# Optimization experiments

Measured on AMD Instinct MI355X. Metric: run time of the kernel, lower is better.

The kernel has to match this reference:

```python
import jax, jax.numpy as jnp
import numpy as np

N_NODES = 100000
N_EDGES = 1600000
D_IN = 128
D_HID = 128
N_GRAPHS = 128


def setup_inputs() -> dict:
    key = jax.random.key(0)
    ks = jax.random.split(key, 6)
    x = jax.random.normal(ks[0], (N_NODES, D_IN), dtype=jnp.float32)
    edge_index = jax.random.randint(ks[1], (2, N_EDGES), 0, N_NODES, dtype=jnp.int32)
    batch = jnp.sort(jax.random.randint(ks[2], (N_NODES,), 0, N_GRAPHS, dtype=jnp.int32))
    # GCNConv params (glorot-ish weight, zero bias), PReLU slope init 0.25 per channel
    W = jax.random.normal(ks[3], (D_IN, D_HID), dtype=jnp.float32) / np.float32(np.sqrt(D_IN))
    b = jnp.zeros((D_HID,), dtype=jnp.float32)
    prelu_a = jnp.full((D_HID,), 0.25, dtype=jnp.float32)
    return {"x": x, "edge_index": edge_index, "batch": batch, "W": W, "b": b, "prelu_a": prelu_a}


def reference(x, edge_index, batch, W, b, prelu_a):
    n_nodes = x.shape[0]
    # ---- GCNConv: add self-loops, symmetric deg^-1/2 normalization ----
    h = x @ W  # [N, H]
    loop = jnp.arange(n_nodes, dtype=edge_index.dtype)
    src = jnp.concatenate([edge_index[0], loop])  # [E+N]
    dst = jnp.concatenate([edge_index[1], loop])
    deg = jax.ops.segment_sum(jnp.ones_like(dst, jnp.float32), dst, num_segments=n_nodes)
    dinv = jnp.where(deg > 0, jax.lax.rsqrt(deg), 0.0)  # deg^-1/2 (inf -> 0, as in PyG)
    norm = dinv[src] * dinv[dst]  # [E+N]
    msg = h[src] * norm[:, None]  # gather + scale
    out = jax.ops.segment_sum(msg, dst, num_segments=n_nodes) + b  # scatter-add
    # ---- PReLU (per-channel slope) ----
    out = jnp.where(out > 0, out, prelu_a * out)
    # ---- F.normalize: L2 over dim=1, eps=1e-12 ----
    nrm = jnp.sqrt(jnp.sum(out * out, axis=1, keepdims=True))
    out = out / jnp.maximum(nrm, 1e-12)
    # ---- global_mean_pool over batch ids ----
    cnt = jax.ops.segment_sum(jnp.ones((n_nodes,), jnp.float32), batch, num_segments=N_GRAPHS)
    pooled = jax.ops.segment_sum(out, batch, num_segments=N_GRAPHS) / jnp.maximum(cnt, 1.0)[:, None]
    return pooled  # [N_GRAPHS, D_HID]
```

## Files before the change

### kernel.cpp

```cpp
#include <hip/hip_runtime.h>

#define D 128
#define NG 128
#define CAP 64
#define BIN 128
#define EPB 4096
#define NBMAX 1024

typedef unsigned short ushort_t;
typedef __bf16 bf16x8 __attribute__((ext_vector_type(8)));
typedef float floatx4 __attribute__((ext_vector_type(4)));

static __device__ __forceinline__ unsigned short f2bf(float f) {
    unsigned u = __float_as_uint(f);
    unsigned r = (u + 0x7fffu + ((u >> 16) & 1u)) >> 16;
    return (unsigned short)r;
}
static __device__ __forceinline__ void acc2(float2& a, unsigned v) {
    a.x += __uint_as_float(v << 16);
    a.y += __uint_as_float(v & 0xffff0000u);
}

__global__ __launch_bounds__(256) void k_init(const float* __restrict__ W, ushort_t* __restrict__ Wp,
                                              const int* __restrict__ batch, int N,
                                              float* __restrict__ cntinv, float* __restrict__ out,
                                              int* __restrict__ cursor, int nb, int cap,
                                              ushort_t* __restrict__ h) {
    int t = blockIdx.x * 256 + threadIdx.x;
    int T = gridDim.x * 256;
    for (int i = t; i < NG * D; i += T) out[i] = 0.f;
    for (int b = t; b < nb; b += T) cursor[b] = b * cap;
    for (int i = t; i < D; i += T) h[(size_t)N * D + i] = 0;
    if (blockIdx.x == 0) {
        int tid = threadIdx.x;
        for (int i = tid; i < D * D; i += 256) {
            int c = i >> 7, k = i & 127;
            Wp[i] = f2bf(W[k * D + c]);
        }
        if (tid < NG) {
            int g = tid;
            int lo = 0, hi = N;
            while (lo < hi) { int mid = (lo + hi) >> 1; if (batch[mid] < g) lo = mid + 1; else hi = mid; }
            int a = lo;
            hi = N;
            while (lo < hi) { int mid = (lo + hi) >> 1; if (batch[mid] < g + 1) lo = mid + 1; else hi = mid; }
            int c = lo - a;
            cntinv[g] = 1.0f / (float)(c > 1 ? c : 1);
        }
    }
}

__global__ __launch_bounds__(256) void k_ascatter(const int* __restrict__ src, const int* __restrict__ dst,
                                                  int E, int nb, int* __restrict__ cursor,
                                                  int* __restrict__ ebuf) {
    __shared__ int hist[NBMAX];
    __shared__ int curs[NBMAX];
    int tid = threadIdx.x;
    for (int i = tid; i < nb; i += 256) hist[i] = 0;
    __syncthreads();
    int base = blockIdx.x * EPB;
    int cnt = E - base; if (cnt > EPB) cnt = EPB;
    for (int k = tid; k < cnt; k += 256) {
        atomicAdd(&hist[(unsigned)dst[base + k] >> 7], 1);
    }
    __syncthreads();
    for (int i = tid; i < nb; i += 256) {
        int v = hist[i];
        curs[i] = v ? atomicAdd(&cursor[i], v) : 0;
    }
    __syncthreads();
    for (int k = tid; k < cnt; k += 256) {
        int dv = dst[base + k];
        int sv = src[base + k];
        int pos = atomicAdd(&curs[dv >> 7], 1);
        ebuf[pos] = (sv << 7) | ((dv & 127) << 24);
    }
}

__global__ __launch_bounds__(512) void k_bucket(int* __restrict__ ebuf, const int* __restrict__ cursor,
                                                int cap, int N, int* __restrict__ rs, int* __restrict__ deg) {
    __shared__ int lists[BIN * CAP];
    __shared__ int lcnt[BIN];
    __shared__ int lpos[BIN];
    int tid = threadIdx.x;
    int b = blockIdx.x;
    if (tid < BIN) lcnt[tid] = 0;
    __syncthreads();
    int s = b * cap;
    int e = cursor[b];
    for (int i = s + tid; i < e; i += 512) {
        int pk = ebuf[i];
        int n = (unsigned)pk >> 24;
        int pos = atomicAdd(&lcnt[n], 1);
        if (pos < CAP) lists[n * CAP + pos] = pk & 0xFFFFFF;
    }
    __syncthreads();
    int c0 = 0, cp0 = 0;
    if (tid < BIN) {
        c0 = min(lcnt[tid], CAP);
        cp0 = (c0 + 7) & ~7;
        lpos[tid] = cp0;
    }
    __syncthreads();
    for (int off = 1; off < BIN; off <<= 1) {
        int tv = 0;
        if (tid < BIN && tid >= off) tv = lpos[tid - off];
        __syncthreads();
        if (tid < BIN) lpos[tid] += tv;
        __syncthreads();
    }
    int n0 = b * BIN;
    if (tid < BIN) {
        int node = n0 + tid;
        if (node < N) { rs[node] = s + lpos[tid] - cp0; deg[node] = c0; }
    }
    __syncthreads();
    {
        int n = tid >> 2, hf = tid & 3;
        int c = min(lcnt[n], CAP);
        int cp = (c + 7) & ~7;
        int wbase = s + lpos[n] - cp;
        for (int k = hf; k < cp; k += 4) {
            ebuf[wbase + k] = (k < c) ? (lists[n * CAP + k] << 1) : (N << 8);
        }
    }
}

__global__ __launch_bounds__(256) void k_gemm(const float* __restrict__ x, const ushort_t* __restrict__ Wp,
                                              const int* __restrict__ deg, ushort_t* __restrict__ h, int N) {
    __shared__ ushort_t smem[64 * 132 + 128 * 128];
    ushort_t* xs = smem;
    ushort_t* ws = smem + 64 * 132;

    const int tid = threadIdx.x;
    const int w = tid >> 6;
    const int lane = tid & 63;
    const int q = lane >> 4;
    const int m = lane & 15;
    const int row0 = blockIdx.x * 64;

#pragma unroll
    for (int it = 0; it < 8; ++it) {
        int i = it * 256 + tid;
        int r = i >> 5, s = i & 31;
        int row = row0 + r;
        uint2 pk;
        if (row < N) {
            float4 v = *(const float4*)&x[(size_t)row * D + s * 4];
            pk.x = (unsigned)f2bf(v.x) | ((unsigned)f2bf(v.y) << 16);
            pk.y = (unsigned)f2bf(v.z) | ((unsigned)f2bf(v.w) << 16);
        } else {
            pk.x = 0; pk.y = 0;
        }
        int off = (s * 8) ^ ((r & 7) << 4);
        *(uint2*)((char*)xs + r * 256 + off) = pk;
    }
#pragma unroll
    for (int it = 0; it < 8; ++it) {
        int i = it * 256 + tid;
        int c = i >> 4, s = i & 15;
        bf16x8 v = *(const bf16x8*)(Wp + (size_t)c * D + s * 8);
        int off = (s * 16) ^ ((c & 7) << 4);
        *(bf16x8*)((char*)ws + c * 256 + off) = v;
    }
    __syncthreads();

    floatx4 acc[8];
#pragma unroll
    for (int nt = 0; nt < 8; ++nt) acc[nt] = (floatx4){0.f, 0.f, 0.f, 0.f};

    const int arow_l = w * 16 + m;
    const int swz = (m & 7) << 4;
#pragma unroll
    for (int kb = 0; kb < 4; ++kb) {
        const int koff = (kb * 64 + q * 16) ^ swz;
        const bf16x8 av = *(const bf16x8*)((const char*)xs + arow_l * 256 + koff);
#pragma unroll
        for (int nt = 0; nt < 8; ++nt) {
            int c = nt * 16 + m;
            const bf16x8 bv = *(const bf16x8*)((const char*)ws + c * 256 + koff);
            acc[nt] = __builtin_amdgcn_mfma_f32_16x16x32_bf16(av, bv, acc[nt], 0, 0, 0);
        }
    }

    float di[4];
#pragma unroll
    for (int r = 0; r < 4; ++r) {
        int row = row0 + w * 16 + q * 4 + r;
        di[r] = (row < N) ? rsqrtf((float)(deg[row] + 1)) : 0.f;
    }
    __syncthreads();

#pragma unroll
    for (int nt = 0; nt < 8; ++nt) {
#pragma unroll
        for (int r = 0; r < 4; ++r) {
            xs[(w * 16 + q * 4 + r) * 132 + nt * 16 + m] = f2bf(acc[nt][r] * di[r]);
        }
    }
    __syncthreads();
#pragma unroll
    for (int it = 0; it < 8; ++it) {
        int i = it * 256 + tid;
        int r = i >> 5, s = i & 31;
        int row = row0 + r;
        if (row < N) {
            *(uint2*)&h[(size_t)row * D + s * 4] = *(const uint2*)&xs[r * 132 + s * 4];
        }
    }
}

__global__ __launch_bounds__(256) void k_gather(const ushort_t* __restrict__ h,
                                                const int* __restrict__ rs, const int* __restrict__ deg,
                                                const int* __restrict__ ebuf,
                                                const int* __restrict__ batch, const float* __restrict__ b,
                                                const float* __restrict__ pa, const float* __restrict__ cntinv,
                                                float* __restrict__ out, int N) {
    __shared__ float rows[8][128];
    __shared__ int gids[8];
    const int wave = threadIdx.x >> 6;
    const int lane = threadIdx.x & 63;
    const int half = lane >> 5;
    const int fl = lane & 31;
    const int hb = half << 5;
    const int node = blockIdx.x * 8 + wave * 2 + half;
    const bool valid = (node < N);
    const int nodeC = valid ? node : (N - 1);
    const char* hp = (const char*)h;
    const unsigned flb = (unsigned)fl * 8;

    float2 a01 = {0.f, 0.f}, a23 = {0.f, 0.f};

    int start = rs[nodeC];
    int len = valid ? deg[nodeC] : 0;
    int lenp = (len + 7) & ~7;

    unsigned idxA = (fl < lenp) ? (unsigned)ebuf[start + fl] : 0;
    int j1 = lenp < 32 ? lenp : 32;
    for (int j = 0; j < j1; j += 8) {
        unsigned o0 = __shfl(idxA, hb + j + 0) + flb;
        unsigned o1 = __shfl(idxA, hb + j + 1) + flb;
        unsigned o2 = __shfl(idxA, hb + j + 2) + flb;
        unsigned o3 = __shfl(idxA, hb + j + 3) + flb;
        unsigned o4 = __shfl(idxA, hb + j + 4) + flb;
        unsigned o5 = __shfl(idxA, hb + j + 5) + flb;
        unsigned o6 = __shfl(idxA, hb + j + 6) + flb;
        unsigned o7 = __shfl(idxA, hb + j + 7) + flb;
        uint2 v0 = *(const uint2*)(hp + o0);
        uint2 v1 = *(const uint2*)(hp + o1);
        uint2 v2 = *(const uint2*)(hp + o2);
        uint2 v3 = *(const uint2*)(hp + o3);
        uint2 v4 = *(const uint2*)(hp + o4);
        uint2 v5 = *(const uint2*)(hp + o5);
        uint2 v6 = *(const uint2*)(hp + o6);
        uint2 v7 = *(const uint2*)(hp + o7);
        acc2(a01, v0.x); acc2(a23, v0.y);
        acc2(a01, v1.x); acc2(a23, v1.y);
        acc2(a01, v2.x); acc2(a23, v2.y);
        acc2(a01, v3.x); acc2(a23, v3.y);
        acc2(a01, v4.x); acc2(a23, v4.y);
        acc2(a01, v5.x); acc2(a23, v5.y);
        acc2(a01, v6.x); acc2(a23, v6.y);
        acc2(a01, v7.x); acc2(a23, v7.y);
    }
    if (lenp > 32) {
        unsigned idxB = (32 + fl < lenp) ? (unsigned)ebuf[start + 32 + fl] : 0;
        for (int j = 32; j < lenp; j += 8) {
            unsigned o0 = __shfl(idxB, hb + j - 32 + 0) + flb;
            unsigned o1 = __shfl(idxB, hb + j - 32 + 1) + flb;
            unsigned o2 = __shfl(idxB, hb + j - 32 + 2) + flb;
            unsigned o3 = __shfl(idxB, hb + j - 32 + 3) + flb;
            unsigned o4 = __shfl(idxB, hb + j - 32 + 4) + flb;
            unsigned o5 = __shfl(idxB, hb + j - 32 + 5) + flb;
            unsigned o6 = __shfl(idxB, hb + j - 32 + 6) + flb;
            unsigned o7 = __shfl(idxB, hb + j - 32 + 7) + flb;
            uint2 v0 = *(const uint2*)(hp + o0);
            uint2 v1 = *(const uint2*)(hp + o1);
            uint2 v2 = *(const uint2*)(hp + o2);
            uint2 v3 = *(const uint2*)(hp + o3);
            uint2 v4 = *(const uint2*)(hp + o4);
            uint2 v5 = *(const uint2*)(hp + o5);
            uint2 v6 = *(const uint2*)(hp + o6);
            uint2 v7 = *(const uint2*)(hp + o7);
            acc2(a01, v0.x); acc2(a23, v0.y);
            acc2(a01, v1.x); acc2(a23, v1.y);
            acc2(a01, v2.x); acc2(a23, v2.y);
            acc2(a01, v3.x); acc2(a23, v3.y);
            acc2(a01, v4.x); acc2(a23, v4.y);
            acc2(a01, v5.x); acc2(a23, v5.y);
            acc2(a01, v6.x); acc2(a23, v6.y);
            acc2(a01, v7.x); acc2(a23, v7.y);
        }
    }

    uint2 sv = *(const uint2*)(hp + (unsigned)nodeC * 256 + flb);
    acc2(a01, sv.x); acc2(a23, sv.y);

    float dinv = rsqrtf((float)(len + 1));
    float4 bb = *(const float4*)&b[fl * 4];
    float4 aa = *(const float4*)&pa[fl * 4];
    float v0 = a01.x * dinv + bb.x;
    float v1 = a01.y * dinv + bb.y;
    float v2 = a23.x * dinv + bb.z;
    float v3 = a23.y * dinv + bb.w;
    v0 = v0 > 0.f ? v0 : aa.x * v0;
    v1 = v1 > 0.f ? v1 : aa.y * v1;
    v2 = v2 > 0.f ? v2 : aa.z * v2;
    v3 = v3 > 0.f ? v3 : aa.w * v3;
    float ss = v0 * v0 + v1 * v1 + v2 * v2 + v3 * v3;
#pragma unroll
    for (int o = 16; o > 0; o >>= 1) ss += __shfl_xor(ss, o);
    float inv = valid ? (1.0f / fmaxf(sqrtf(ss), 1e-12f)) : 0.f;

    *(float4*)&rows[wave * 2 + half][fl * 4] = make_float4(v0 * inv, v1 * inv, v2 * inv, v3 * inv);
    if (fl == 0) gids[wave * 2 + half] = valid ? batch[node] : -1;
    __syncthreads();

    if (threadIdx.x < 128) {
        int f = threadIdx.x;
        float acc = rows[0][f];
        int g = gids[0];
#pragma unroll
        for (int i = 1; i < 8; ++i) {
            int gi = gids[i];
            float vv = rows[i][f];
            if (gi == g) {
                acc += vv;
            } else {
                if (g >= 0) atomicAdd(&out[(size_t)g * D + f], acc * cntinv[g]);
                g = gi;
                acc = vv;
            }
        }
        if (g >= 0) atomicAdd(&out[(size_t)g * D + f], acc * cntinv[g]);
    }
}

extern "C" void kernel_launch(void* const* d_in, const int* in_sizes, int n_in,
                              void* d_out, int out_size, void* d_ws, size_t ws_size,
                              hipStream_t stream) {
    const float* x = (const float*)d_in[0];
    const int* ei = (const int*)d_in[1];
    const int* batch = (const int*)d_in[2];
    const float* W = (const float*)d_in[3];
    const float* b = (const float*)d_in[4];
    const float* pa = (const float*)d_in[5];
    float* out = (float*)d_out;

    const int N = in_sizes[0] / D;
    const int E = in_sizes[1] / 2;
    const int* src = ei;
    const int* dst = ei + E;

    const int nb = (N + BIN - 1) / BIN;
    const int nblk = (E + EPB - 1) / EPB;
    const int mean = (E + nb - 1) / nb;
    const int cap = mean + mean / 2 + 640;

    char* w = (char*)d_ws;
    auto carve = [&](size_t bytes) {
        void* p = (void*)w;
        w += (bytes + 255) & ~(size_t)255;
        return p;
    };
    ushort_t* h = (ushort_t*)carve((size_t)(N + 1) * D * sizeof(ushort_t));
    ushort_t* Wp = (ushort_t*)carve((size_t)D * D * sizeof(ushort_t));
    int* deg = (int*)carve((size_t)N * sizeof(int));
    int* rs = (int*)carve((size_t)N * sizeof(int));
    int* ebuf = (int*)carve((size_t)nb * cap * sizeof(int));
    int* cursor = (int*)carve(NBMAX * sizeof(int));
    float* cntinv = (float*)carve(NG * sizeof(float));

    k_init<<<32, 256, 0, stream>>>(W, Wp, batch, N, cntinv, out, cursor, nb, cap, h);
    k_ascatter<<<nblk, 256, 0, stream>>>(src, dst, E, nb, cursor, ebuf);
    k_bucket<<<nb, 512, 0, stream>>>(ebuf, cursor, cap, N, rs, deg);
    k_gemm<<<(N + 63) / 64, 256, 0, stream>>>(x, Wp, deg, h, N);
    k_gather<<<(N + 7) / 8, 256, 0, stream>>>(h, rs, deg, ebuf, batch, b, pa, cntinv, out, N);
}
```

Measured before the change: 223.2 us.

## Fuse bucket sort and GEMM into one kernel, compute degrees via atomics

Degree counting moves into the edge-scatter pass through global atomics, so the GEMM no longer depends on the bucket kernel. The bucket and GEMM work are then merged into a single launch, with blocks interleaved between the two roles, letting them overlap. The gather loop is unrolled to 16 loads per step, and the gather is split into two launches. The cost is 1.6M extra global atomics on deg and larger shared-memory pressure for the bucket blocks, which now run 256 threads instead of 512.

```diff
diff --git a/kernel.cpp b/kernel.cpp
--- a/kernel.cpp
+++ b/kernel.cpp
@@ -24,10 +24,11 @@
 __global__ __launch_bounds__(256) void k_init(const float* __restrict__ W, ushort_t* __restrict__ Wp,
                                               const int* __restrict__ batch, int N,
                                               float* __restrict__ cntinv, float* __restrict__ out,
-                                              int* __restrict__ cursor, int nb, int cap,
-                                              ushort_t* __restrict__ h) {
+                                              int* __restrict__ cursor, int* __restrict__ deg,
+                                              int nb, int cap, ushort_t* __restrict__ h) {
     int t = blockIdx.x * 256 + threadIdx.x;
     int T = gridDim.x * 256;
+    for (int i = t; i < N; i += T) deg[i] = 0;
     for (int i = t; i < NG * D; i += T) out[i] = 0.f;
     for (int b = t; b < nb; b += T) cursor[b] = b * cap;
     for (int i = t; i < D; i += T) h[(size_t)N * D + i] = 0;
@@ -52,7 +53,7 @@
 
 __global__ __launch_bounds__(256) void k_ascatter(const int* __restrict__ src, const int* __restrict__ dst,
                                                   int E, int nb, int* __restrict__ cursor,
-                                                  int* __restrict__ ebuf) {
+                                                  int* __restrict__ ebuf, int* __restrict__ deg) {
     __shared__ int hist[NBMAX];
     __shared__ int curs[NBMAX];
     int tid = threadIdx.x;
@@ -61,7 +62,9 @@
     int base = blockIdx.x * EPB;
     int cnt = E - base; if (cnt > EPB) cnt = EPB;
     for (int k = tid; k < cnt; k += 256) {
-        atomicAdd(&hist[(unsigned)dst[base + k] >> 7], 1);
+        int dv = dst[base + k];
+        atomicAdd(&hist[(unsigned)dv >> 7], 1);
+        atomicAdd(&deg[dv], 1);
     }
     __syncthreads();
     for (int i = tid; i < nb; i += 256) {
@@ -77,135 +80,139 @@
     }
 }
 
-__global__ __launch_bounds__(512) void k_bucket(int* __restrict__ ebuf, const int* __restrict__ cursor,
-                                                int cap, int N, int* __restrict__ rs, int* __restrict__ deg) {
-    __shared__ int lists[BIN * CAP];
-    __shared__ int lcnt[BIN];
-    __shared__ int lpos[BIN];
-    int tid = threadIdx.x;
-    int b = blockIdx.x;
-    if (tid < BIN) lcnt[tid] = 0;
-    __syncthreads();
-    int s = b * cap;
-    int e = cursor[b];
-    for (int i = s + tid; i < e; i += 512) {
-        int pk = ebuf[i];
-        int n = (unsigned)pk >> 24;
-        int pos = atomicAdd(&lcnt[n], 1);
-        if (pos < CAP) lists[n * CAP + pos] = pk & 0xFFFFFF;
-    }
-    __syncthreads();
-    int c0 = 0, cp0 = 0;
-    if (tid < BIN) {
-        c0 = min(lcnt[tid], CAP);
-        cp0 = (c0 + 7) & ~7;
-        lpos[tid] = cp0;
-    }
-    __syncthreads();
-    for (int off = 1; off < BIN; off <<= 1) {
-        int tv = 0;
-        if (tid < BIN && tid >= off) tv = lpos[tid - off];
-        __syncthreads();
-        if (tid < BIN) lpos[tid] += tv;
-        __syncthreads();
-    }
-    int n0 = b * BIN;
-    if (tid < BIN) {
-        int node = n0 + tid;
-        if (node < N) { rs[node] = s + lpos[tid] - cp0; deg[node] = c0; }
-    }
-    __syncthreads();
-    {
-        int n = tid >> 2, hf = tid & 3;
-        int c = min(lcnt[n], CAP);
-        int cp = (c + 7) & ~7;
-        int wbase = s + lpos[n] - cp;
-        for (int k = hf; k < cp; k += 4) {
-            ebuf[wbase + k] = (k < c) ? (lists[n * CAP + k] << 1) : (N << 8);
-        }
-    }
-}
-
-__global__ __launch_bounds__(256) void k_gemm(const float* __restrict__ x, const ushort_t* __restrict__ Wp,
-                                              const int* __restrict__ deg, ushort_t* __restrict__ h, int N) {
-    __shared__ ushort_t smem[64 * 132 + 128 * 128];
-    ushort_t* xs = smem;
-    ushort_t* ws = smem + 64 * 132;
-
+__global__ __launch_bounds__(256) void k_mid(const float* __restrict__ x, const ushort_t* __restrict__ Wp,
+                                             const int* __restrict__ deg, ushort_t* __restrict__ h,
+                                             int* __restrict__ ebuf, const int* __restrict__ cursor,
+                                             int cap, int* __restrict__ rs, int N,
+                                             int nbBucket, int total) {
+    __shared__ __align__(16) char smemraw[(64 * 132 + 128 * 128) * 2];
     const int tid = threadIdx.x;
-    const int w = tid >> 6;
-    const int lane = tid & 63;
-    const int q = lane >> 4;
-    const int m = lane & 15;
-    const int row0 = blockIdx.x * 64;
-
-#pragma unroll
-    for (int it = 0; it < 8; ++it) {
-        int i = it * 256 + tid;
-        int r = i >> 5, s = i & 31;
-        int row = row0 + r;
-        uint2 pk;
-        if (row < N) {
-            float4 v = *(const float4*)&x[(size_t)row * D + s * 4];
-            pk.x = (unsigned)f2bf(v.x) | ((unsigned)f2bf(v.y) << 16);
-            pk.y = (unsigned)f2bf(v.z) | ((unsigned)f2bf(v.w) << 16);
-        } else {
-            pk.x = 0; pk.y = 0;
-        }
-        int off = (s * 8) ^ ((r & 7) << 4);
-        *(uint2*)((char*)xs + r * 256 + off) = pk;
-    }
-#pragma unroll
-    for (int it = 0; it < 8; ++it) {
-        int i = it * 256 + tid;
-        int c = i >> 4, s = i & 15;
-        bf16x8 v = *(const bf16x8*)(Wp + (size_t)c * D + s * 8);
-        int off = (s * 16) ^ ((c & 7) << 4);
-        *(bf16x8*)((char*)ws + c * 256 + off) = v;
-    }
-    __syncthreads();
-
-    floatx4 acc[8];
-#pragma unroll
-    for (int nt = 0; nt < 8; ++nt) acc[nt] = (floatx4){0.f, 0.f, 0.f, 0.f};
-
-    const int arow_l = w * 16 + m;
-    const int swz = (m & 7) << 4;
-#pragma unroll
-    for (int kb = 0; kb < 4; ++kb) {
-        const int koff = (kb * 64 + q * 16) ^ swz;
-        const bf16x8 av = *(const bf16x8*)((const char*)xs + arow_l * 256 + koff);
+    const int idx = blockIdx.x;
+    const int bIdx = (int)(((long)idx * nbBucket) / total);
+    const bool isB = (((long)(idx + 1) * nbBucket) / total) > bIdx;
+
+    if (isB) {
+        int* lists = (int*)smemraw;
+        int* lcnt = lists + BIN * CAP;
+        int* lpos = lcnt + BIN;
+        int b = bIdx;
+        if (tid < BIN) lcnt[tid] = 0;
+        __syncthreads();
+        int s = b * cap;
+        int e = cursor[b];
+        for (int i = s + tid; i < e; i += 256) {
+            int pk = ebuf[i];
+            int n = (unsigned)pk >> 24;
+            int pos = atomicAdd(&lcnt[n], 1);
+            if (pos < CAP) lists[n * CAP + pos] = pk & 0xFFFFFF;
+        }
+        __syncthreads();
+        int c0 = 0, cp0 = 0;
+        if (tid < BIN) {
+            c0 = min(lcnt[tid], CAP);
+            cp0 = (c0 + 7) & ~7;
+            lpos[tid] = cp0;
+        }
+        __syncthreads();
+        for (int off = 1; off < BIN; off <<= 1) {
+            int tv = 0;
+            if (tid < BIN && tid >= off) tv = lpos[tid - off];
+            __syncthreads();
+            if (tid < BIN) lpos[tid] += tv;
+            __syncthreads();
+        }
+        int n0 = b * BIN;
+        if (tid < BIN) {
+            int node = n0 + tid;
+            if (node < N) rs[node] = s + lpos[tid] - cp0;
+        }
+        __syncthreads();
+        {
+            int n = tid >> 1, hf = tid & 1;
+            int c = min(lcnt[n], CAP);
+            int cp = (c + 7) & ~7;
+            int wbase = s + lpos[n] - cp;
+            for (int k = hf; k < cp; k += 2) {
+                ebuf[wbase + k] = (k < c) ? (lists[n * CAP + k] << 1) : (N << 8);
+            }
+        }
+    } else {
+        ushort_t* xs = (ushort_t*)smemraw;
+        ushort_t* ws = (ushort_t*)smemraw + 64 * 132;
+        const int w = tid >> 6;
+        const int lane = tid & 63;
+        const int q = lane >> 4;
+        const int m = lane & 15;
+        const int row0 = (idx - bIdx) * 64;
+
+#pragma unroll
+        for (int it = 0; it < 8; ++it) {
+            int i = it * 256 + tid;
+            int r = i >> 5, s = i & 31;
+            int row = row0 + r;
+            uint2 pk;
+            if (row < N) {
+                float4 v = *(const float4*)&x[(size_t)row * D + s * 4];
+                pk.x = (unsigned)f2bf(v.x) | ((unsigned)f2bf(v.y) << 16);
+                pk.y = (unsigned)f2bf(v.z) | ((unsigned)f2bf(v.w) << 16);
+            } else {
+                pk.x = 0; pk.y = 0;
+            }
+            int off = (s * 8) ^ ((r & 7) << 4);
+            *(uint2*)((char*)xs + r * 256 + off) = pk;
+        }
+#pragma unroll
+        for (int it = 0; it < 8; ++it) {
+            int i = it * 256 + tid;
+            int c = i >> 4, s = i & 15;
+            bf16x8 v = *(const bf16x8*)(Wp + (size_t)c * D + s * 8);
+            int off = (s * 16) ^ ((c & 7) << 4);
+            *(bf16x8*)((char*)ws + c * 256 + off) = v;
+        }
+        __syncthreads();
+
+        floatx4 acc[8];
+#pragma unroll
+        for (int nt = 0; nt < 8; ++nt) acc[nt] = (floatx4){0.f, 0.f, 0.f, 0.f};
+
+        const int arow_l = w * 16 + m;
+        const int swz = (m & 7) << 4;
+#pragma unroll
+        for (int kb = 0; kb < 4; ++kb) {
+            const int koff = (kb * 64 + q * 16) ^ swz;
+            const bf16x8 av = *(const bf16x8*)((const char*)xs + arow_l * 256 + koff);
+#pragma unroll
+            for (int nt = 0; nt < 8; ++nt) {
+                int c = nt * 16 + m;
+                const bf16x8 bv = *(const bf16x8*)((const char*)ws + c * 256 + koff);
+                acc[nt] = __builtin_amdgcn_mfma_f32_16x16x32_bf16(av, bv, acc[nt], 0, 0, 0);
+            }
+        }
+
+        float di[4];
+#pragma unroll
+        for (int r = 0; r < 4; ++r) {
+            int row = row0 + w * 16 + q * 4 + r;
+            di[r] = (row < N) ? rsqrtf((float)(min(deg[row], CAP) + 1)) : 0.f;
+        }
+        __syncthreads();
+
 #pragma unroll
         for (int nt = 0; nt < 8; ++nt) {
-            int c = nt * 16 + m;
-            const bf16x8 bv = *(const bf16x8*)((const char*)ws + c * 256 + koff);
-            acc[nt] = __builtin_amdgcn_mfma_f32_16x16x32_bf16(av, bv, acc[nt], 0, 0, 0);
-        }
-    }
-
-    float di[4];
-#pragma unroll
-    for (int r = 0; r < 4; ++r) {
-        int row = row0 + w * 16 + q * 4 + r;
-        di[r] = (row < N) ? rsqrtf((float)(deg[row] + 1)) : 0.f;
-    }
-    __syncthreads();
-
-#pragma unroll
-    for (int nt = 0; nt < 8; ++nt) {
-#pragma unroll
-        for (int r = 0; r < 4; ++r) {
-            xs[(w * 16 + q * 4 + r) * 132 + nt * 16 + m] = f2bf(acc[nt][r] * di[r]);
-        }
-    }
-    __syncthreads();
-#pragma unroll
-    for (int it = 0; it < 8; ++it) {
-        int i = it * 256 + tid;
-        int r = i >> 5, s = i & 31;
-        int row = row0 + r;
-        if (row < N) {
-            *(uint2*)&h[(size_t)row * D + s * 4] = *(const uint2*)&xs[r * 132 + s * 4];
+#pragma unroll
+            for (int r = 0; r < 4; ++r) {
+                xs[(w * 16 + q * 4 + r) * 132 + nt * 16 + m] = f2bf(acc[nt][r] * di[r]);
+            }
+        }
+        __syncthreads();
+#pragma unroll
+        for (int it = 0; it < 8; ++it) {
+            int i = it * 256 + tid;
+            int r = i >> 5, s = i & 31;
+            int row = row0 + r;
+            if (row < N) {
+                *(uint2*)&h[(size_t)row * D + s * 4] = *(const uint2*)&xs[r * 132 + s * 4];
+            }
         }
     }
 }
@@ -215,7 +222,7 @@
                                                 const int* __restrict__ ebuf,
                                                 const int* __restrict__ batch, const float* __restrict__ b,
                                                 const float* __restrict__ pa, const float* __restrict__ cntinv,
-                                                float* __restrict__ out, int N) {
+                                                float* __restrict__ out, int nodeBase, int N) {
     __shared__ float rows[8][128];
     __shared__ int gids[8];
     const int wave = threadIdx.x >> 6;
@@ -223,7 +230,7 @@
     const int half = lane >> 5;
     const int fl = lane & 31;
     const int hb = half << 5;
-    const int node = blockIdx.x * 8 + wave * 2 + half;
+    const int node = nodeBase + blockIdx.x * 8 + wave * 2 + half;
     const bool valid = (node < N);
     const int nodeC = valid ? node : (N - 1);
     const char* hp = (const char*)h;
@@ -232,64 +239,43 @@
     float2 a01 = {0.f, 0.f}, a23 = {0.f, 0.f};
 
     int start = rs[nodeC];
-    int len = valid ? deg[nodeC] : 0;
+    int len = valid ? min(deg[nodeC], CAP) : 0;
     int lenp = (len + 7) & ~7;
 
     unsigned idxA = (fl < lenp) ? (unsigned)ebuf[start + fl] : 0;
-    int j1 = lenp < 32 ? lenp : 32;
-    for (int j = 0; j < j1; j += 8) {
-        unsigned o0 = __shfl(idxA, hb + j + 0) + flb;
-        unsigned o1 = __shfl(idxA, hb + j + 1) + flb;
-        unsigned o2 = __shfl(idxA, hb + j + 2) + flb;
-        unsigned o3 = __shfl(idxA, hb + j + 3) + flb;
-        unsigned o4 = __shfl(idxA, hb + j + 4) + flb;
-        unsigned o5 = __shfl(idxA, hb + j + 5) + flb;
-        unsigned o6 = __shfl(idxA, hb + j + 6) + flb;
-        unsigned o7 = __shfl(idxA, hb + j + 7) + flb;
-        uint2 v0 = *(const uint2*)(hp + o0);
-        uint2 v1 = *(const uint2*)(hp + o1);
-        uint2 v2 = *(const uint2*)(hp + o2);
-        uint2 v3 = *(const uint2*)(hp + o3);
-        uint2 v4 = *(const uint2*)(hp + o4);
-        uint2 v5 = *(const uint2*)(hp + o5);
-        uint2 v6 = *(const uint2*)(hp + o6);
-        uint2 v7 = *(const uint2*)(hp + o7);
-        acc2(a01, v0.x); acc2(a23, v0.y);
-        acc2(a01, v1.x); acc2(a23, v1.y);
-        acc2(a01, v2.x); acc2(a23, v2.y);
-        acc2(a01, v3.x); acc2(a23, v3.y);
-        acc2(a01, v4.x); acc2(a23, v4.y);
-        acc2(a01, v5.x); acc2(a23, v5.y);
-        acc2(a01, v6.x); acc2(a23, v6.y);
-        acc2(a01, v7.x); acc2(a23, v7.y);
+    int lA = lenp < 32 ? lenp : 32;
+    int j = 0;
+    for (; j + 16 <= lA; j += 16) {
+        unsigned o[16];
+        uint2 v[16];
+#pragma unroll
+        for (int t = 0; t < 16; ++t) o[t] = __shfl(idxA, hb + j + t) + flb;
+#pragma unroll
+        for (int t = 0; t < 16; ++t) v[t] = *(const uint2*)(hp + o[t]);
+#pragma unroll
+        for (int t = 0; t < 16; ++t) { acc2(a01, v[t].x); acc2(a23, v[t].y); }
+    }
+    if (j < lA) {
+        unsigned o[8];
+        uint2 v[8];
+#pragma unroll
+        for (int t = 0; t < 8; ++t) o[t] = __shfl(idxA, hb + j + t) + flb;
+#pragma unroll
+        for (int t = 0; t < 8; ++t) v[t] = *(const uint2*)(hp + o[t]);
+#pragma unroll
+        for (int t = 0; t < 8; ++t) { acc2(a01, v[t].x); acc2(a23, v[t].y); }
     }
     if (lenp > 32) {
         unsigned idxB = (32 + fl < lenp) ? (unsigned)ebuf[start + 32 + fl] : 0;
-        for (int j = 32; j < lenp; j += 8) {
-            unsigned o0 = __shfl(idxB, hb + j - 32 + 0) + flb;
-            unsigned o1 = __shfl(idxB, hb + j - 32 + 1) + flb;
-            unsigned o2 = __shfl(idxB, hb + j - 32 + 2) + flb;
-            unsigned o3 = __shfl(idxB, hb + j - 32 + 3) + flb;
-            unsigned o4 = __shfl(idxB, hb + j - 32 + 4) + flb;
-            unsigned o5 = __shfl(idxB, hb + j - 32 + 5) + flb;
-            unsigned o6 = __shfl(idxB, hb + j - 32 + 6) + flb;
-            unsigned o7 = __shfl(idxB, hb + j - 32 + 7) + flb;
-            uint2 v0 = *(const uint2*)(hp + o0);
-            uint2 v1 = *(const uint2*)(hp + o1);
-            uint2 v2 = *(const uint2*)(hp + o2);
-            uint2 v3 = *(const uint2*)(hp + o3);
-            uint2 v4 = *(const uint2*)(hp + o4);
-            uint2 v5 = *(const uint2*)(hp + o5);
-            uint2 v6 = *(const uint2*)(hp + o6);
-            uint2 v7 = *(const uint2*)(hp + o7);
-            acc2(a01, v0.x); acc2(a23, v0.y);
-            acc2(a01, v1.x); acc2(a23, v1.y);
-            acc2(a01, v2.x); acc2(a23, v2.y);
-            acc2(a01, v3.x); acc2(a23, v3.y);
-            acc2(a01, v4.x); acc2(a23, v4.y);
-            acc2(a01, v5.x); acc2(a23, v5.y);
-            acc2(a01, v6.x); acc2(a23, v6.y);
-            acc2(a01, v7.x); acc2(a23, v7.y);
+        for (int jj = 32; jj < lenp; jj += 8) {
+            unsigned o[8];
+            uint2 v[8];
+#pragma unroll
+            for (int t = 0; t < 8; ++t) o[t] = __shfl(idxB, hb + jj - 32 + t) + flb;
+#pragma unroll
+            for (int t = 0; t < 8; ++t) v[t] = *(const uint2*)(hp + o[t]);
+#pragma unroll
+            for (int t = 0; t < 8; ++t) { acc2(a01, v[t].x); acc2(a23, v[t].y); }
         }
     }
 
@@ -356,6 +342,8 @@
     const int nblk = (E + EPB - 1) / EPB;
     const int mean = (E + nb - 1) / nb;
     const int cap = mean + mean / 2 + 640;
+    const int gb = (N + 63) / 64;
+    const int midTotal = gb + nb;
 
     char* w = (char*)d_ws;
     auto carve = [&](size_t bytes) {
@@ -371,9 +359,14 @@
     int* cursor = (int*)carve(NBMAX * sizeof(int));
     float* cntinv = (float*)carve(NG * sizeof(float));
 
-    k_init<<<32, 256, 0, stream>>>(W, Wp, batch, N, cntinv, out, cursor, nb, cap, h);
-    k_ascatter<<<nblk, 256, 0, stream>>>(src, dst, E, nb, cursor, ebuf);
-    k_bucket<<<nb, 512, 0, stream>>>(ebuf, cursor, cap, N, rs, deg);
-    k_gemm<<<(N + 63) / 64, 256, 0, stream>>>(x, Wp, deg, h, N);
-    k_gather<<<(N + 7) / 8, 256, 0, stream>>>(h, rs, deg, ebuf, batch, b, pa, cntinv, out, N);
-}
+    k_init<<<32, 256, 0, stream>>>(W, Wp, batch, N, cntinv, out, cursor, deg, nb, cap, h);
+    k_ascatter<<<nblk, 256, 0, stream>>>(src, dst, E, nb, cursor, ebuf, deg);
+    k_mid<<<midTotal, 256, 0, stream>>>(x, Wp, deg, h, ebuf, cursor, cap, rs, N, nb, midTotal);
+    {
+        int blocksTot = (N + 7) / 8;
+        int blocks1 = blocksTot / 2;
+        k_gather<<<blocks1, 256, 0, stream>>>(h, rs, deg, ebuf, batch, b, pa, cntinv, out, 0, N);
+        k_gather<<<blocksTot - blocks1, 256, 0, stream>>>(h, rs, deg, ebuf, batch, b, pa, cntinv, out,
+                                                          blocks1 * 8, N);
+    }
+}
```

Result: slower. 295.2 us (+32.3%).

## Fuse edge bucketing and GEMM into one kernel per 128-node bin

Applied to the files above, without the earlier changes.

Merges the per-bin edge bucketing kernel with the dense x@W GEMM so that each block of 512 threads bins edges for 128 nodes, then computes h for those same 128 rows, reusing shared memory and reading degrees from LDS instead of global memory. This removes one kernel launch and the global round trip of deg between stages. The trade-off is fewer, larger blocks (about 782 instead of 1563 GEMM blocks) with large shared memory use, which can lower occupancy and serialise the bucketing phase with the GEMM inside each block.

```diff
diff --git a/kernel.cpp b/kernel.cpp
--- a/kernel.cpp
+++ b/kernel.cpp
@@ -77,13 +77,22 @@
     }
 }
 
-__global__ __launch_bounds__(512) void k_bucket(int* __restrict__ ebuf, const int* __restrict__ cursor,
-                                                int cap, int N, int* __restrict__ rs, int* __restrict__ deg) {
-    __shared__ int lists[BIN * CAP];
+__global__ __launch_bounds__(512) void k_fuse(const float* __restrict__ x, const ushort_t* __restrict__ Wp,
+                                              int* __restrict__ ebuf, const int* __restrict__ cursor,
+                                              int cap, int N, int* __restrict__ rs, int* __restrict__ deg,
+                                              ushort_t* __restrict__ h) {
+    __shared__ __align__(16) char smem[128 * 132 * 2 + 128 * 128 * 2];
     __shared__ int lcnt[BIN];
     __shared__ int lpos[BIN];
-    int tid = threadIdx.x;
-    int b = blockIdx.x;
+    __shared__ int sdeg[BIN];
+    int* lists = (int*)smem;
+    ushort_t* xs = (ushort_t*)smem;
+    ushort_t* ws = (ushort_t*)(smem + 128 * 132 * 2);
+
+    const int tid = threadIdx.x;
+    const int b = blockIdx.x;
+    const int row0 = b * BIN;
+
     if (tid < BIN) lcnt[tid] = 0;
     __syncthreads();
     int s = b * cap;
@@ -100,6 +109,7 @@
         c0 = min(lcnt[tid], CAP);
         cp0 = (c0 + 7) & ~7;
         lpos[tid] = cp0;
+        sdeg[tid] = c0;
     }
     __syncthreads();
     for (int off = 1; off < BIN; off <<= 1) {
@@ -109,9 +119,8 @@
         if (tid < BIN) lpos[tid] += tv;
         __syncthreads();
     }
-    int n0 = b * BIN;
     if (tid < BIN) {
-        int node = n0 + tid;
+        int node = row0 + tid;
         if (node < N) { rs[node] = s + lpos[tid] - cp0; deg[node] = c0; }
     }
     __syncthreads();
@@ -124,43 +133,35 @@
             ebuf[wbase + k] = (k < c) ? (lists[n * CAP + k] << 1) : (N << 8);
         }
     }
-}
-
-__global__ __launch_bounds__(256) void k_gemm(const float* __restrict__ x, const ushort_t* __restrict__ Wp,
-                                              const int* __restrict__ deg, ushort_t* __restrict__ h, int N) {
-    __shared__ ushort_t smem[64 * 132 + 128 * 128];
-    ushort_t* xs = smem;
-    ushort_t* ws = smem + 64 * 132;
-
-    const int tid = threadIdx.x;
+    __syncthreads();
+
     const int w = tid >> 6;
     const int lane = tid & 63;
     const int q = lane >> 4;
     const int m = lane & 15;
-    const int row0 = blockIdx.x * 64;
 
 #pragma unroll
     for (int it = 0; it < 8; ++it) {
-        int i = it * 256 + tid;
-        int r = i >> 5, s = i & 31;
+        int i = it * 512 + tid;
+        int r = i >> 5, sc = i & 31;
         int row = row0 + r;
         uint2 pk;
         if (row < N) {
-            float4 v = *(const float4*)&x[(size_t)row * D + s * 4];
+            float4 v = *(const float4*)&x[(size_t)row * D + sc * 4];
             pk.x = (unsigned)f2bf(v.x) | ((unsigned)f2bf(v.y) << 16);
             pk.y = (unsigned)f2bf(v.z) | ((unsigned)f2bf(v.w) << 16);
         } else {
             pk.x = 0; pk.y = 0;
         }
-        int off = (s * 8) ^ ((r & 7) << 4);
+        int off = (sc * 8) ^ ((r & 7) << 4);
         *(uint2*)((char*)xs + r * 256 + off) = pk;
     }
 #pragma unroll
-    for (int it = 0; it < 8; ++it) {
-        int i = it * 256 + tid;
-        int c = i >> 4, s = i & 15;
-        bf16x8 v = *(const bf16x8*)(Wp + (size_t)c * D + s * 8);
-        int off = (s * 16) ^ ((c & 7) << 4);
+    for (int it = 0; it < 4; ++it) {
+        int i = it * 512 + tid;
+        int c = i >> 4, sc = i & 15;
+        bf16x8 v = *(const bf16x8*)(Wp + (size_t)c * D + sc * 8);
+        int off = (sc * 16) ^ ((c & 7) << 4);
         *(bf16x8*)((char*)ws + c * 256 + off) = v;
     }
     __syncthreads();
@@ -186,8 +187,8 @@
     float di[4];
 #pragma unroll
     for (int r = 0; r < 4; ++r) {
-        int row = row0 + w * 16 + q * 4 + r;
-        di[r] = (row < N) ? rsqrtf((float)(deg[row] + 1)) : 0.f;
+        int rr = w * 16 + q * 4 + r;
+        di[r] = (row0 + rr < N) ? rsqrtf((float)(sdeg[rr] + 1)) : 0.f;
     }
     __syncthreads();
 
@@ -201,11 +202,11 @@
     __syncthreads();
 #pragma unroll
     for (int it = 0; it < 8; ++it) {
-        int i = it * 256 + tid;
-        int r = i >> 5, s = i & 31;
+        int i = it * 512 + tid;
+        int r = i >> 5, sc = i & 31;
         int row = row0 + r;
         if (row < N) {
-            *(uint2*)&h[(size_t)row * D + s * 4] = *(const uint2*)&xs[r * 132 + s * 4];
+            *(uint2*)&h[(size_t)row * D + sc * 4] = *(const uint2*)&xs[r * 132 + sc * 4];
         }
     }
 }
@@ -373,7 +374,6 @@
 
     k_init<<<32, 256, 0, stream>>>(W, Wp, batch, N, cntinv, out, cursor, nb, cap, h);
     k_ascatter<<<nblk, 256, 0, stream>>>(src, dst, E, nb, cursor, ebuf);
-    k_bucket<<<nb, 512, 0, stream>>>(ebuf, cursor, cap, N, rs, deg);
-    k_gemm<<<(N + 63) / 64, 256, 0, stream>>>(x, Wp, deg, h, N);
+    k_fuse<<<nb, 512, 0, stream>>>(x, Wp, ebuf, cursor, cap, N, rs, deg, h);
     k_gather<<<(N + 7) / 8, 256, 0, stream>>>(h, rs, deg, ebuf, batch, b, pa, cntinv, out, N);
 }
```

Result: no change. 220.3 us (-1.3%).
